# Kernel tuning notes

Measured on AMD Instinct MI355X. Metric: run time of the kernel, lower is better.

## Reference

```python
import jax, jax.numpy as jnp
import numpy as np

VERY_NEGATIVE_NUMBER = -1e29

B, TC, TQ, D = 32, 2048, 256, 256


def setup_inputs() -> dict:
    key = jax.random.key(0)
    k1, k2, k3, k4 = jax.random.split(key, 4)
    context_repr = jax.random.normal(k1, (B, TC, D), dtype=jnp.float32)
    question_repr = jax.random.normal(k2, (B, TQ, D), dtype=jnp.float32)
    # lengths in [1, maxlen] so no row is fully masked
    context_len = jax.random.randint(k3, (B,), 1, TC + 1, dtype=jnp.int32)
    question_len = jax.random.randint(k4, (B,), 1, TQ + 1, dtype=jnp.int32)
    return {
        "context_repr": context_repr,
        "question_repr": question_repr,
        "context_len": context_len,
        "question_len": question_len,
    }


def reference(context_repr, question_repr, context_len, question_len):
    dtype = context_repr.dtype
    Tc = context_repr.shape[1]
    Tq = question_repr.shape[1]
    # similarity: dot product over feature dim -> [B, Tc, Tq]
    sim_mat = jnp.einsum("bcd,bqd->bcq", context_repr, question_repr)
    # sequence masks
    cmask = (jnp.arange(Tc)[None, :] < context_len[:, None]).astype(dtype)  # [B,Tc]
    qmask = (jnp.arange(Tq)[None, :] < question_len[:, None]).astype(dtype)  # [B,Tq]
    mask = cmask[:, :, None] * qmask[:, None, :]  # [B,Tc,Tq]
    sim_mat = sim_mat + (1.0 - mask) * VERY_NEGATIVE_NUMBER
    # context-to-query attention
    c2q_prob = jax.nn.softmax(sim_mat, axis=-1)  # [B,Tc,Tq]
    context2query_attention = jnp.einsum("bcq,bqd->bcd", c2q_prob, question_repr)
    # query-to-context attention: row-wise max then softmax over context positions
    q2c_prob = jax.nn.softmax(jnp.max(sim_mat, axis=-1), axis=-1)  # [B,Tc]
    q2c = jnp.einsum("bc,bcd->bd", q2c_prob, context_repr)  # [B,D]
    query2context_attention = jnp.broadcast_to(
        q2c[:, None, :], context2query_attention.shape
    )
    return (context2query_attention, query2context_attention)
```

## Files before the change

### kernel.cpp

```cpp
#include <hip/hip_runtime.h>
#include <hip/hip_fp16.h>

#define DEVI __device__ __forceinline__

typedef float f32x4 __attribute__((ext_vector_type(4)));
typedef float float4v __attribute__((ext_vector_type(4)));
typedef _Float16 f16x8 __attribute__((ext_vector_type(8)));
typedef unsigned short us8 __attribute__((ext_vector_type(8)));

constexpr int NB = 32, TC = 2048, TQ = 256, DD = 256;
constexpr int CR = 64;
constexpr float VNEG = -1e29f;

DEVI unsigned short f2h(float f) {
  _Float16 h = (_Float16)f;
  return __builtin_bit_cast(unsigned short, h);
}
DEVI float h2f(unsigned short u) {
  return (float)__builtin_bit_cast(_Float16, u);
}

DEVI int swz(int row, int cb) { return cb ^ (((row ^ (cb >> 7)) & 7) << 4); }

DEVI f32x4 mfmah(us8 a, us8 b, f32x4 c) {
  return __builtin_amdgcn_mfma_f32_16x16x32_f16(
      __builtin_bit_cast(f16x8, a), __builtin_bit_cast(f16x8, b), c, 0, 0, 0);
}

__global__ void P0(const float* __restrict__ Qg, unsigned short* __restrict__ Qh,
                   unsigned short* __restrict__ QT)
{
  __shared__ unsigned short t[64][72];
  const int bid = blockIdx.x, tid = threadIdx.x;
  const int b = bid >> 4;
  const int q0 = ((bid >> 2) & 3) * 64, d0 = (bid & 3) * 64;
  {
    const int qr = tid >> 2, dp = (tid & 3) * 16;
    const float* src = Qg + ((size_t)b * TQ + q0 + qr) * DD + d0 + dp;
    unsigned short* dst = Qh + ((size_t)b * TQ + q0 + qr) * DD + d0 + dp;
    us8 o0, o1;
#pragma unroll
    for (int i = 0; i < 4; ++i) {
      float4v v = *(const float4v*)(src + i * 4);
#pragma unroll
      for (int j = 0; j < 4; ++j) {
        const unsigned short h = f2h(v[j]);
        t[qr][dp + i * 4 + j] = h;
        if (i < 2) o0[i * 4 + j] = h; else o1[(i - 2) * 4 + j] = h;
      }
    }
    *(us8*)dst = o0;
    *(us8*)(dst + 8) = o1;
  }
  __syncthreads();
  {
    const int dr = tid >> 2, qp = (tid & 3) * 16;
    us8 a, c;
#pragma unroll
    for (int i = 0; i < 8; ++i) a[i] = t[qp + i][dr];
#pragma unroll
    for (int i = 0; i < 8; ++i) c[i] = t[qp + 8 + i][dr];
    unsigned short* dst = QT + ((size_t)b * DD + d0 + dr) * TQ + q0 + qp;
    *(us8*)dst = a;
    *(us8*)(dst + 8) = c;
  }
}

__global__ __launch_bounds__(512, 6)
void kA(const float* __restrict__ Cg, const unsigned short* __restrict__ Qh,
        const unsigned short* __restrict__ QT,
        const int* __restrict__ clenp, const int* __restrict__ qlenp,
        float* __restrict__ out1, float* __restrict__ pnum,
        float* __restrict__ ptM, float* __restrict__ ptD)
{
  __shared__ __align__(16) char lds[32768];
  __shared__ float redM[512];
  __shared__ float redS[512];
  __shared__ float wred[64];
  __shared__ float wexp[64];
  __shared__ float sinv[64];
  char* const bufC = lds;
  char* const bufP = lds;

  const int bid = blockIdx.x;
  const int b = bid & 31;
  const int tile = bid >> 5;
  const int c0 = tile * CR;
  const int tid = threadIdx.x;
  const int l = tid & 63, wid = tid >> 6;
  const int g = l >> 4, lm = l & 15;
  const int clen = clenp[b], qlen = qlenp[b];

  const float* Cb = Cg + (size_t)(b * TC + c0) * DD;
  const unsigned short* Qhb = Qh + (size_t)b * TQ * DD;
  const unsigned short* QTb = QT + (size_t)b * DD * TQ;

  {
    const int r = tid >> 3;
    const int d0 = (tid & 7) * 32;
    const float* src = Cb + (size_t)r * DD + d0;
#pragma unroll
    for (int i = 0; i < 4; ++i) {
      us8 h;
#pragma unroll
      for (int k = 0; k < 8; k += 4) {
        float4v v = *(const float4v*)(src + i * 8 + k);
#pragma unroll
        for (int j = 0; j < 4; ++j) h[k + j] = f2h(v[j]);
      }
      *(us8*)(bufC + r * 512 + swz(r, (d0 + i * 8) * 2)) = h;
    }
  }
  __syncthreads();

  f32x4 acc[4][2];
#pragma unroll
  for (int mt = 0; mt < 4; ++mt)
#pragma unroll
    for (int nt = 0; nt < 2; ++nt) acc[mt][nt] = (f32x4)0.0f;

  us8 bh[2][2];
#pragma unroll
  for (int nt = 0; nt < 2; ++nt)
    bh[0][nt] = *(const us8*)(Qhb + (size_t)(wid * 32 + nt * 16 + lm) * DD + g * 8);
#pragma unroll
  for (int kk = 0; kk < 8; ++kk) {
    const int cur = kk & 1, nxt = cur ^ 1;
    if (kk < 7) {
#pragma unroll
      for (int nt = 0; nt < 2; ++nt)
        bh[nxt][nt] = *(const us8*)(Qhb + (size_t)(wid * 32 + nt * 16 + lm) * DD +
                                    (kk + 1) * 32 + g * 8);
    }
    us8 ah[4];
#pragma unroll
    for (int mt = 0; mt < 4; ++mt) {
      const int row = mt * 16 + lm;
      ah[mt] = *(const us8*)(bufC + row * 512 + swz(row, kk * 64 + g * 16));
    }
#pragma unroll
    for (int mt = 0; mt < 4; ++mt)
#pragma unroll
      for (int nt = 0; nt < 2; ++nt)
        acc[mt][nt] = mfmah(ah[mt], bh[cur][nt], acc[mt][nt]);
  }

#pragma unroll
  for (int nt = 0; nt < 2; ++nt) {
    const int q = wid * 32 + nt * 16 + lm;
    const bool qm = q >= qlen;
#pragma unroll
    for (int mt = 0; mt < 4; ++mt)
#pragma unroll
      for (int j = 0; j < 4; ++j) {
        const int c = c0 + mt * 16 + g * 4 + j;
        if (qm || c >= clen) acc[mt][nt][j] = VNEG;
      }
  }

#pragma unroll
  for (int mt = 0; mt < 4; ++mt)
#pragma unroll
    for (int j = 0; j < 4; ++j) {
      float m = fmaxf(acc[mt][0][j], acc[mt][1][j]);
      m = fmaxf(m, __shfl_xor(m, 1, 64));
      m = fmaxf(m, __shfl_xor(m, 2, 64));
      m = fmaxf(m, __shfl_xor(m, 4, 64));
      m = fmaxf(m, __shfl_xor(m, 8, 64));
      if (lm == 0) redM[wid * 64 + mt * 16 + g * 4 + j] = m;
    }
  __syncthreads();

  if (tid < 64) {
    float m = redM[tid];
#pragma unroll
    for (int w = 1; w < 8; ++w) m = fmaxf(m, redM[w * 64 + tid]);
    wred[tid] = m;
  }
  __syncthreads();

#pragma unroll
  for (int mt = 0; mt < 4; ++mt)
#pragma unroll
    for (int j = 0; j < 4; ++j) {
      const float m = wred[mt * 16 + g * 4 + j];
      float s = 0.f;
#pragma unroll
      for (int nt = 0; nt < 2; ++nt) {
        const float p = __expf(acc[mt][nt][j] - m);
        acc[mt][nt][j] = p;
        s += p;
      }
      s += __shfl_xor(s, 1, 64);
      s += __shfl_xor(s, 2, 64);
      s += __shfl_xor(s, 4, 64);
      s += __shfl_xor(s, 8, 64);
      if (lm == 0) redS[wid * 64 + mt * 16 + g * 4 + j] = s;
    }
  if (wid == 0) {
    float m = wred[l];
    m = fmaxf(m, __shfl_xor(m, 1, 64));  m = fmaxf(m, __shfl_xor(m, 2, 64));
    m = fmaxf(m, __shfl_xor(m, 4, 64));  m = fmaxf(m, __shfl_xor(m, 8, 64));
    m = fmaxf(m, __shfl_xor(m, 16, 64)); m = fmaxf(m, __shfl_xor(m, 32, 64));
    const float wv = __expf(wred[l] - m);
    wexp[l] = wv;
    float s = wv;
    s += __shfl_xor(s, 1, 64);  s += __shfl_xor(s, 2, 64);
    s += __shfl_xor(s, 4, 64);  s += __shfl_xor(s, 8, 64);
    s += __shfl_xor(s, 16, 64); s += __shfl_xor(s, 32, 64);
    if (l == 0) { ptD[b * 32 + tile] = s; ptM[b * 32 + tile] = m; }
  }
  __syncthreads();

  if (tid < 64) {
    float s = 0.f;
#pragma unroll
    for (int w = 0; w < 8; ++w) s += redS[w * 64 + tid];
    sinv[tid] = 1.0f / s;
  }

  {
    const int half = tid >> 8;
    const int d = tid & 255;
    float qacc = 0.f;
    const int d2 = d * 2;
#pragma unroll 8
    for (int r = half * 32; r < half * 32 + 32; ++r) {
      const float cv = h2f(*(const unsigned short*)(bufC + r * 512 + swz(r, d2)));
      qacc += wexp[r] * cv;
    }
    pnum[(((size_t)b * 32 + tile) * 2 + half) * DD + d] = qacc;
  }
  __syncthreads();

#pragma unroll
  for (int mt = 0; mt < 4; ++mt)
#pragma unroll
    for (int nt = 0; nt < 2; ++nt)
#pragma unroll
      for (int j = 0; j < 4; ++j) {
        const int row = mt * 16 + g * 4 + j;
        const int cb = (wid * 32 + nt * 16 + lm) * 2;
        *(unsigned short*)(bufP + row * 512 + swz(row, cb)) = f2h(acc[mt][nt][j]);
      }
  __syncthreads();

  f32x4 pacc[4][2];
#pragma unroll
  for (int mt = 0; mt < 4; ++mt)
#pragma unroll
    for (int dt = 0; dt < 2; ++dt) pacc[mt][dt] = (f32x4)0.0f;

  us8 qb[2][2];
#pragma unroll
  for (int dt = 0; dt < 2; ++dt)
    qb[0][dt] = *(const us8*)(QTb + (size_t)(wid * 32 + dt * 16 + lm) * TQ + g * 8);
#pragma unroll
  for (int kq = 0; kq < 8; ++kq) {
    const int cur = kq & 1, nxt = cur ^ 1;
    if (kq < 7) {
#pragma unroll
      for (int dt = 0; dt < 2; ++dt)
        qb[nxt][dt] = *(const us8*)(QTb + (size_t)(wid * 32 + dt * 16 + lm) * TQ +
                                    (kq + 1) * 32 + g * 8);
    }
    us8 pa[4];
#pragma unroll
    for (int mt = 0; mt < 4; ++mt) {
      const int row = mt * 16 + lm;
      pa[mt] = *(const us8*)(bufP + row * 512 + swz(row, kq * 64 + g * 16));
    }
#pragma unroll
    for (int mt = 0; mt < 4; ++mt)
#pragma unroll
      for (int dt = 0; dt < 2; ++dt)
        pacc[mt][dt] = mfmah(pa[mt], qb[cur][dt], pacc[mt][dt]);
  }

#pragma unroll
  for (int mt = 0; mt < 4; ++mt)
#pragma unroll
    for (int j = 0; j < 4; ++j) {
      const int row = mt * 16 + g * 4 + j;
      const float inv = sinv[row];
      const size_t rowoff = (size_t)(b * TC + c0 + row) * DD;
#pragma unroll
      for (int dt = 0; dt < 2; ++dt)
        out1[rowoff + wid * 32 + dt * 16 + lm] = pacc[mt][dt][j] * inv;
    }
}

__global__ void kC(const float* __restrict__ pnum, const float* __restrict__ ptM,
                   const float* __restrict__ ptD, float* __restrict__ out2)
{
  const int b = blockIdx.x >> 4, seg = blockIdx.x & 15;
  const int d = threadIdx.x;
  __shared__ float sM[32], sD[32];
  if (d < 32) { sM[d] = ptM[b * 32 + d]; sD[d] = ptD[b * 32 + d]; }
  __syncthreads();
  float m = sM[0];
#pragma unroll
  for (int t = 1; t < 32; ++t) m = fmaxf(m, sM[t]);
  float den = 0.f, acc = 0.f;
#pragma unroll
  for (int t = 0; t < 32; ++t) {
    const float sc = __expf(sM[t] - m);
    den += sc * sD[t];
    const size_t base = (((size_t)b * 32 + t) * 2) * DD + d;
    acc += sc * (pnum[base] + pnum[base + DD]);
  }
  const float s = acc / den;
  float* dst = out2 + ((size_t)b * TC + seg * 128) * DD + d;
#pragma unroll 4
  for (int c = 0; c < 128; ++c) dst[(size_t)c * DD] = s;
}

extern "C" void kernel_launch(void* const* d_in, const int* in_sizes, int n_in,
                              void* d_out, int out_size, void* d_ws, size_t ws_size,
                              hipStream_t stream)
{
  const float* Cg = (const float*)d_in[0];
  const float* Qg = (const float*)d_in[1];
  const int* clen = (const int*)d_in[2];
  const int* qlen = (const int*)d_in[3];
  float* out1 = (float*)d_out;
  float* out2 = out1 + (size_t)NB * TC * DD;

  char* ws = (char*)d_ws;
  float* pnum = (float*)(ws);
  float* ptM  = (float*)(ws + 2097152);
  float* ptD  = (float*)(ws + 2101248);
  unsigned short* Qh = (unsigned short*)(ws + 2105344);
  unsigned short* QT = (unsigned short*)(ws + 2105344 + 4194304);

  P0 <<<dim3(512), dim3(256), 0, stream>>>(Qg, Qh, QT);
  kA <<<dim3(NB * (TC / CR)), dim3(512), 0, stream>>>(Cg, Qh, QT, clen, qlen,
                                                      out1, pnum, ptM, ptD);
  kC <<<dim3(NB * 16), dim3(256), 0, stream>>>(pnum, ptM, ptD, out2);
}
```

Measured before the change: 83.03 us.

## Skip masked context tiles and query chunks using precomputed question mean

```diff
diff --git a/kernel.cpp b/kernel.cpp
--- a/kernel.cpp
+++ b/kernel.cpp
@@ -28,47 +28,56 @@
 }
 
 __global__ void P0(const float* __restrict__ Qg, unsigned short* __restrict__ Qh,
-                   unsigned short* __restrict__ QT)
+                   unsigned short* __restrict__ QT, float* __restrict__ qmean)
 {
   __shared__ unsigned short t[64][72];
   const int bid = blockIdx.x, tid = threadIdx.x;
-  const int b = bid >> 4;
-  const int q0 = ((bid >> 2) & 3) * 64, d0 = (bid & 3) * 64;
-  {
-    const int qr = tid >> 2, dp = (tid & 3) * 16;
-    const float* src = Qg + ((size_t)b * TQ + q0 + qr) * DD + d0 + dp;
-    unsigned short* dst = Qh + ((size_t)b * TQ + q0 + qr) * DD + d0 + dp;
-    us8 o0, o1;
-#pragma unroll
-    for (int i = 0; i < 4; ++i) {
-      float4v v = *(const float4v*)(src + i * 4);
-#pragma unroll
-      for (int j = 0; j < 4; ++j) {
-        const unsigned short h = f2h(v[j]);
-        t[qr][dp + i * 4 + j] = h;
-        if (i < 2) o0[i * 4 + j] = h; else o1[(i - 2) * 4 + j] = h;
-      }
-    }
-    *(us8*)dst = o0;
-    *(us8*)(dst + 8) = o1;
-  }
-  __syncthreads();
-  {
-    const int dr = tid >> 2, qp = (tid & 3) * 16;
-    us8 a, c;
-#pragma unroll
-    for (int i = 0; i < 8; ++i) a[i] = t[qp + i][dr];
-#pragma unroll
-    for (int i = 0; i < 8; ++i) c[i] = t[qp + 8 + i][dr];
-    unsigned short* dst = QT + ((size_t)b * DD + d0 + dr) * TQ + q0 + qp;
-    *(us8*)dst = a;
-    *(us8*)(dst + 8) = c;
+  if (bid < 512) {
+    const int b = bid >> 4;
+    const int q0 = ((bid >> 2) & 3) * 64, d0 = (bid & 3) * 64;
+    {
+      const int qr = tid >> 2, dp = (tid & 3) * 16;
+      const float* src = Qg + ((size_t)b * TQ + q0 + qr) * DD + d0 + dp;
+      unsigned short* dst = Qh + ((size_t)b * TQ + q0 + qr) * DD + d0 + dp;
+      us8 o0, o1;
+#pragma unroll
+      for (int i = 0; i < 4; ++i) {
+        float4v v = *(const float4v*)(src + i * 4);
+#pragma unroll
+        for (int j = 0; j < 4; ++j) {
+          const unsigned short h = f2h(v[j]);
+          t[qr][dp + i * 4 + j] = h;
+          if (i < 2) o0[i * 4 + j] = h; else o1[(i - 2) * 4 + j] = h;
+        }
+      }
+      *(us8*)dst = o0;
+      *(us8*)(dst + 8) = o1;
+    }
+    __syncthreads();
+    {
+      const int dr = tid >> 2, qp = (tid & 3) * 16;
+      us8 a, c;
+#pragma unroll
+      for (int i = 0; i < 8; ++i) a[i] = t[qp + i][dr];
+#pragma unroll
+      for (int i = 0; i < 8; ++i) c[i] = t[qp + 8 + i][dr];
+      unsigned short* dst = QT + ((size_t)b * DD + d0 + dr) * TQ + q0 + qp;
+      *(us8*)dst = a;
+      *(us8*)(dst + 8) = c;
+    }
+  } else {
+    const int b = bid - 512;
+    const float* src = Qg + (size_t)b * TQ * DD + tid;
+    float s = 0.f;
+#pragma unroll 8
+    for (int q = 0; q < TQ; ++q) s += src[(size_t)q * DD];
+    qmean[b * DD + tid] = s * (1.0f / 256.0f);
   }
 }
 
 __global__ __launch_bounds__(512, 6)
 void kA(const float* __restrict__ Cg, const unsigned short* __restrict__ Qh,
-        const unsigned short* __restrict__ QT,
+        const unsigned short* __restrict__ QT, const float* __restrict__ qmean,
         const int* __restrict__ clenp, const int* __restrict__ qlenp,
         float* __restrict__ out1, float* __restrict__ pnum,
         float* __restrict__ ptM, float* __restrict__ ptD)
@@ -83,22 +92,39 @@
   char* const bufP = lds;
 
   const int bid = blockIdx.x;
-  const int b = bid & 31;
-  const int tile = bid >> 5;
+  const int b = bid >> 5;
+  const int tile = bid & 31;
   const int c0 = tile * CR;
   const int tid = threadIdx.x;
+  const int clen = clenp[b], qlen = qlenp[b];
+
+  if (c0 >= clen) {
+    const int r = tid >> 3;
+    const int d0 = (tid & 7) * 32;
+    const float* qm = qmean + b * DD + d0;
+    float4v v[8];
+#pragma unroll
+    for (int i = 0; i < 8; ++i) v[i] = *(const float4v*)(qm + i * 4);
+    float* dst = out1 + (size_t)(b * TC + c0 + r) * DD + d0;
+#pragma unroll
+    for (int i = 0; i < 8; ++i) *(float4v*)(dst + i * 4) = v[i];
+    pnum[(((size_t)b * 32 + tile) * 2 + (tid >> 8)) * DD + (tid & 255)] = 0.f;
+    if (tid == 0) { ptM[b * 32 + tile] = VNEG; ptD[b * 32 + tile] = 0.f; }
+    return;
+  }
+
   const int l = tid & 63, wid = tid >> 6;
   const int g = l >> 4, lm = l & 15;
-  const int clen = clenp[b], qlen = qlenp[b];
-
-  const float* Cb = Cg + (size_t)(b * TC + c0) * DD;
+  const bool wq_active = (wid * 32 < qlen);
+  const int kqmax = (qlen + 31) >> 5;
+
   const unsigned short* Qhb = Qh + (size_t)b * TQ * DD;
   const unsigned short* QTb = QT + (size_t)b * DD * TQ;
 
   {
     const int r = tid >> 3;
     const int d0 = (tid & 7) * 32;
-    const float* src = Cb + (size_t)r * DD + d0;
+    const float* src = Cg + (size_t)(b * TC + c0 + r) * DD + d0;
 #pragma unroll
     for (int i = 0; i < 4; ++i) {
       us8 h;
@@ -119,30 +145,32 @@
 #pragma unroll
     for (int nt = 0; nt < 2; ++nt) acc[mt][nt] = (f32x4)0.0f;
 
-  us8 bh[2][2];
-#pragma unroll
-  for (int nt = 0; nt < 2; ++nt)
-    bh[0][nt] = *(const us8*)(Qhb + (size_t)(wid * 32 + nt * 16 + lm) * DD + g * 8);
-#pragma unroll
-  for (int kk = 0; kk < 8; ++kk) {
-    const int cur = kk & 1, nxt = cur ^ 1;
-    if (kk < 7) {
-#pragma unroll
-      for (int nt = 0; nt < 2; ++nt)
-        bh[nxt][nt] = *(const us8*)(Qhb + (size_t)(wid * 32 + nt * 16 + lm) * DD +
-                                    (kk + 1) * 32 + g * 8);
-    }
-    us8 ah[4];
-#pragma unroll
-    for (int mt = 0; mt < 4; ++mt) {
-      const int row = mt * 16 + lm;
-      ah[mt] = *(const us8*)(bufC + row * 512 + swz(row, kk * 64 + g * 16));
-    }
-#pragma unroll
-    for (int mt = 0; mt < 4; ++mt)
-#pragma unroll
-      for (int nt = 0; nt < 2; ++nt)
-        acc[mt][nt] = mfmah(ah[mt], bh[cur][nt], acc[mt][nt]);
+  if (wq_active) {
+    us8 bh[2][2];
+#pragma unroll
+    for (int nt = 0; nt < 2; ++nt)
+      bh[0][nt] = *(const us8*)(Qhb + (size_t)(wid * 32 + nt * 16 + lm) * DD + g * 8);
+#pragma unroll
+    for (int kk = 0; kk < 8; ++kk) {
+      const int cur = kk & 1, nxt = cur ^ 1;
+      if (kk < 7) {
+#pragma unroll
+        for (int nt = 0; nt < 2; ++nt)
+          bh[nxt][nt] = *(const us8*)(Qhb + (size_t)(wid * 32 + nt * 16 + lm) * DD +
+                                      (kk + 1) * 32 + g * 8);
+      }
+      us8 ah[4];
+#pragma unroll
+      for (int mt = 0; mt < 4; ++mt) {
+        const int row = mt * 16 + lm;
+        ah[mt] = *(const us8*)(bufC + row * 512 + swz(row, kk * 64 + g * 16));
+      }
+#pragma unroll
+      for (int mt = 0; mt < 4; ++mt)
+#pragma unroll
+        for (int nt = 0; nt < 2; ++nt)
+          acc[mt][nt] = mfmah(ah[mt], bh[cur][nt], acc[mt][nt]);
+    }
   }
 
 #pragma unroll
@@ -233,60 +261,71 @@
   }
   __syncthreads();
 
-#pragma unroll
-  for (int mt = 0; mt < 4; ++mt)
-#pragma unroll
-    for (int nt = 0; nt < 2; ++nt)
-#pragma unroll
-      for (int j = 0; j < 4; ++j) {
-        const int row = mt * 16 + g * 4 + j;
-        const int cb = (wid * 32 + nt * 16 + lm) * 2;
-        *(unsigned short*)(bufP + row * 512 + swz(row, cb)) = f2h(acc[mt][nt][j]);
-      }
-  __syncthreads();
+  if (wq_active) {
+#pragma unroll
+    for (int mt = 0; mt < 4; ++mt)
+#pragma unroll
+      for (int nt = 0; nt < 2; ++nt)
+#pragma unroll
+        for (int j = 0; j < 4; ++j) {
+          const int row = mt * 16 + g * 4 + j;
+          const int cb = (wid * 32 + nt * 16 + lm) * 2;
+          *(unsigned short*)(bufP + row * 512 + swz(row, cb)) = f2h(acc[mt][nt][j]);
+        }
+  }
+  __syncthreads();
+
+  us8 qt[16];
+#pragma unroll
+  for (int kq = 0; kq < 8; ++kq) {
+    if (kq < kqmax) {
+#pragma unroll
+      for (int dt = 0; dt < 2; ++dt)
+        qt[kq * 2 + dt] = *(const us8*)(QTb +
+            (size_t)(wid * 32 + dt * 16 + lm) * TQ + kq * 32 + g * 8);
+    }
+  }
 
   f32x4 pacc[4][2];
 #pragma unroll
   for (int mt = 0; mt < 4; ++mt)
 #pragma unroll
     for (int dt = 0; dt < 2; ++dt) pacc[mt][dt] = (f32x4)0.0f;
-
-  us8 qb[2][2];
-#pragma unroll
-  for (int dt = 0; dt < 2; ++dt)
-    qb[0][dt] = *(const us8*)(QTb + (size_t)(wid * 32 + dt * 16 + lm) * TQ + g * 8);
 #pragma unroll
   for (int kq = 0; kq < 8; ++kq) {
-    const int cur = kq & 1, nxt = cur ^ 1;
-    if (kq < 7) {
-#pragma unroll
-      for (int dt = 0; dt < 2; ++dt)
-        qb[nxt][dt] = *(const us8*)(QTb + (size_t)(wid * 32 + dt * 16 + lm) * TQ +
-                                    (kq + 1) * 32 + g * 8);
-    }
-    us8 pa[4];
-#pragma unroll
-    for (int mt = 0; mt < 4; ++mt) {
-      const int row = mt * 16 + lm;
-      pa[mt] = *(const us8*)(bufP + row * 512 + swz(row, kq * 64 + g * 16));
-    }
-#pragma unroll
-    for (int mt = 0; mt < 4; ++mt)
-#pragma unroll
-      for (int dt = 0; dt < 2; ++dt)
-        pacc[mt][dt] = mfmah(pa[mt], qb[cur][dt], pacc[mt][dt]);
-  }
-
+    if (kq < kqmax) {
+      us8 pa[4];
+#pragma unroll
+      for (int mt = 0; mt < 4; ++mt) {
+        const int row = mt * 16 + lm;
+        pa[mt] = *(const us8*)(bufP + row * 512 + swz(row, kq * 64 + g * 16));
+      }
+#pragma unroll
+      for (int mt = 0; mt < 4; ++mt)
+#pragma unroll
+        for (int dt = 0; dt < 2; ++dt)
+          pacc[mt][dt] = mfmah(pa[mt], qt[kq * 2 + dt], pacc[mt][dt]);
+    }
+  }
+
+  float qv[2];
+  if (clen < c0 + CR) {
+#pragma unroll
+    for (int dt = 0; dt < 2; ++dt)
+      qv[dt] = qmean[b * DD + wid * 32 + dt * 16 + lm];
+  }
 #pragma unroll
   for (int mt = 0; mt < 4; ++mt)
 #pragma unroll
     for (int j = 0; j < 4; ++j) {
       const int row = mt * 16 + g * 4 + j;
       const float inv = sinv[row];
+      const bool valid = (c0 + row) < clen;
       const size_t rowoff = (size_t)(b * TC + c0 + row) * DD;
 #pragma unroll
       for (int dt = 0; dt < 2; ++dt)
-        out1[rowoff + wid * 32 + dt * 16 + lm] = pacc[mt][dt][j] * inv;
+        out1[rowoff + wid * 32 + dt * 16 + lm] =
+            valid ? pacc[mt][dt][j] * inv : qv[dt];
     }
 }
 
@@ -327,14 +366,16 @@
   float* out2 = out1 + (size_t)NB * TC * DD;
 
   char* ws = (char*)d_ws;
-  float* pnum = (float*)(ws);
-  float* ptM  = (float*)(ws + 2097152);
-  float* ptD  = (float*)(ws + 2101248);
-  unsigned short* Qh = (unsigned short*)(ws + 2105344);
-  unsigned short* QT = (unsigned short*)(ws + 2105344 + 4194304);
-
-  P0 <<<dim3(512), dim3(256), 0, stream>>>(Qg, Qh, QT);
-  kA <<<dim3(NB * (TC / CR)), dim3(512), 0, stream>>>(Cg, Qh, QT, clen, qlen,
+  float* pnum  = (float*)(ws);
+  float* ptM   = (float*)(ws + 2097152);
+  float* ptD   = (float*)(ws + 2101248);
+  float* qmean = (float*)(ws + 2105344);
+  unsigned short* Qh = (unsigned short*)(ws + 2138112);
+  unsigned short* QT = (unsigned short*)(ws + 2138112 + 4194304);
+
+  P0 <<<dim3(544), dim3(256), 0, stream>>>(Qg, Qh, QT, qmean);
+  kA <<<dim3(NB * (TC / CR)), dim3(512), 0, stream>>>(Cg, Qh, QT, qmean,
+                                                      clen, qlen,
                                                       out1, pnum, ptM, ptD);
   kC <<<dim3(NB * 16), dim3(256), 0, stream>>>(pnum, ptM, ptD, out2);
 }
```

New measurement: 89.38 us. 1.08x slower.
